# Kernel tuning notes

Measured on AMD Instinct MI355X. Metric: run time of the kernel, lower is better.

The kernel has to match this reference:

```python
import jax, jax.numpy as jnp
import numpy as np

B, T, HID = 4, 2048, 1024
H, D = 16, 64  # num_heads, depth = hidden // heads
NEG_INF = -1e9


def setup_inputs() -> dict:
    key = jax.random.key(0)
    ks = jax.random.split(key, 8)
    s = 1.0 / np.sqrt(HID)
    return {
        "q": jax.random.normal(ks[0], (B, T, HID), jnp.float32),
        "k": jax.random.normal(ks[1], (B, T, HID), jnp.float32),
        "v": jax.random.normal(ks[2], (B, T, HID), jnp.float32),
        "pad_mask": jax.random.randint(ks[3], (B, T), 0, 2, jnp.int32),
        "Wq": jax.random.normal(ks[4], (HID, HID), jnp.float32) * s,
        "Wk": jax.random.normal(ks[5], (HID, HID), jnp.float32) * s,
        "Wv": jax.random.normal(ks[6], (HID, HID), jnp.float32) * s,
        "Wo": jax.random.normal(ks[7], (HID, HID), jnp.float32) * s,
    }


def _split_heads(x):
    # [B, T, HID] -> [B*H, T, D]
    b, t, _ = x.shape
    return x.reshape(b, t, H, D).transpose(0, 2, 1, 3).reshape(b * H, t, D)


def _combine_heads(x):
    # [B*H, T, D] -> [B, T, HID]
    t = x.shape[1]
    return x.reshape(-1, H, t, D).transpose(0, 2, 1, 3).reshape(-1, t, HID)


def reference(q, k, v, pad_mask, Wq, Wk, Wv, Wo):
    qp = _split_heads(q @ Wq) * (D ** -0.5)   # [B*H, Tq, D]
    kp = _split_heads(k @ Wk)                  # [B*H, Tk, D]
    vp = _split_heads(v @ Wv)                  # [B*H, Tk, D]
    # additive pad bias: repeat([H,1]) is head-major tiling, reproduced via jnp.tile
    bias = jnp.tile(pad_mask.astype(jnp.float32) * NEG_INF, (H, 1))[:, None, :]
    logits = jnp.einsum('bqd,bkd->bqk', qp, kp) + bias  # [B*H, Tq, Tk]
    weights = jax.nn.softmax(logits, axis=-1)
    # original calls functional.dropout but discards the result -> no-op
    out = jnp.einsum('bqk,bkd->bqd', weights, vp)
    out = _combine_heads(out)                  # [B, Tq, HID]
    return out @ Wo
```

## Files before the change

### kernel.cpp

```cpp
#include <hip/hip_runtime.h>
#include <hip/hip_bf16.h>

#define TQ 2048
#define HIDDEN 1024
#define NB 4
#define NH 16
#define DH 64
#define BHN (NB*NH)
#define LOG2E 1.44269504f

typedef __attribute__((ext_vector_type(4))) float f32x4;
typedef __attribute__((ext_vector_type(8))) short s16x8;

#if __has_builtin(__builtin_amdgcn_exp2f)
#define EXP2(x) __builtin_amdgcn_exp2f(x)
#else
#define EXP2(x) exp2f(x)
#endif

__device__ inline unsigned short f2bf(float f) {
    union { float f; unsigned int u; } x; x.f = f;
    unsigned int r = x.u + 0x7fffu + ((x.u >> 16) & 1u);
    return (unsigned short)(r >> 16);
}

__device__ inline unsigned int pkbf(float a, float b) {
    __hip_bfloat162 h = __float22bfloat162_rn(make_float2(a, b));
    return *reinterpret_cast<unsigned int*>(&h);
}

union PBU { uint4 u4; s16x8 v; };

#define GLL16(gsrc, ldst) \
    __builtin_amdgcn_global_load_lds( \
        (const __attribute__((address_space(1))) unsigned int*)(gsrc), \
        (__attribute__((address_space(3))) unsigned int*)(ldst), 16, 0, 0)

__global__ __launch_bounds__(256) void maskprep(const int* __restrict__ pad,
                                                unsigned short* __restrict__ maskAndB) {
    int p = blockIdx.x * 256 + threadIdx.x;
    int r = p >> 11, off = p & 2047;
    int o6 = off & 63;
    int ks = o6 >> 5, k32 = o6 & 31;
    int lg = k32 >> 3, j = k32 & 7;
    int key = (off & ~63) | (ks * 32 + ((j >> 2) << 4) + (lg << 2) + (j & 3));
    maskAndB[p] = pad[r * 2048 + key] ? (unsigned short)0 : (unsigned short)0xFFFF;
}

__global__ __launch_bounds__(256) void wt_kernel(const float* W0, const float* W1,
                                                 const float* W2, const float* W3,
                                                 unsigned short* Wt) {
    const float* W = (blockIdx.z == 0) ? W0 : (blockIdx.z == 1) ? W1
                    : (blockIdx.z == 2) ? W2 : W3;
    unsigned short* out = Wt + (size_t)blockIdx.z * HIDDEN * HIDDEN;
    __shared__ float tile[64][68];
    int t = threadIdx.x;
    int k0 = blockIdx.y * 64, n0 = blockIdx.x * 64;
#pragma unroll
    for (int i = 0; i < 4; i++) {
        int r = (t >> 4) + i * 16;
        int c = (t & 15) * 4;
        float4 v = *(const float4*)(W + (size_t)(k0 + r) * HIDDEN + n0 + c);
        tile[r][c] = v.x; tile[r][c+1] = v.y; tile[r][c+2] = v.z; tile[r][c+3] = v.w;
    }
    __syncthreads();
#pragma unroll
    for (int i = 0; i < 4; i++) {
        int n = (t >> 4) + i * 16;
        int kc = (t & 15) * 4;
        ushort4 o;
        o.x = f2bf(tile[kc+0][n]); o.y = f2bf(tile[kc+1][n]);
        o.z = f2bf(tile[kc+2][n]); o.w = f2bf(tile[kc+3][n]);
        *(ushort4*)(out + (size_t)(n0 + n) * HIDDEN + k0 + kc) = o;
    }
}

__global__ __launch_bounds__(256) void gemm_proj(const float* __restrict__ A,
                                                 const unsigned short* __restrict__ Bt,
                                                 unsigned short* __restrict__ outb,
                                                 float scale, int vt) {
    __shared__ alignas(16) float As[128 * 32];
    __shared__ alignas(16) unsigned short Bs[128 * 32];
    const int t = threadIdx.x;
    const int wave = t >> 6, lane = t & 63;
    const int wr = wave >> 1, wc = wave & 1;
    const int lr = lane & 15, lg = lane >> 4;
    const int linear = blockIdx.x + 8 * blockIdx.y;
    const int tile = ((linear & 7) << 6) | (linear >> 3);
    const int m0 = (tile >> 3) * 128, n0 = (tile & 7) * 128;

    int fA[4]; size_t gA[4];
#pragma unroll
    for (int i = 0; i < 4; i++) {
        fA[i] = i * 256 + t;
        int row = fA[i] >> 3, sg = (fA[i] & 7) ^ (row & 7);
        gA[i] = (size_t)(m0 + row) * HIDDEN + sg * 4;
    }
    int fB[2]; size_t gB[2];
#pragma unroll
    for (int i = 0; i < 2; i++) {
        fB[i] = i * 256 + t;
        int row = fB[i] >> 2, sg = (fB[i] & 3) ^ (row & 3);
        gB[i] = (size_t)(n0 + row) * HIDDEN + sg * 8;
    }
    float* lA0 = &As[(size_t)(0 * 256 + wave * 64) * 4];
    float* lA1 = &As[(size_t)(1 * 256 + wave * 64) * 4];
    float* lA2 = &As[(size_t)(2 * 256 + wave * 64) * 4];
    float* lA3 = &As[(size_t)(3 * 256 + wave * 64) * 4];
    unsigned short* lB0 = &Bs[(size_t)(0 * 256 + wave * 64) * 8];
    unsigned short* lB1 = &Bs[(size_t)(1 * 256 + wave * 64) * 8];

    f32x4 acc[4][4] = {};

    for (int k0 = 0; k0 < HIDDEN; k0 += 32) {
        __syncthreads();
        GLL16(A + gA[0] + k0, lA0);
        GLL16(A + gA[1] + k0, lA1);
        GLL16(A + gA[2] + k0, lA2);
        GLL16(A + gA[3] + k0, lA3);
        GLL16(Bt + gB[0] + k0, lB0);
        GLL16(Bt + gB[1] + k0, lB1);
        __syncthreads();
        s16x8 af[4], bfr[4];
#pragma unroll
        for (int mi = 0; mi < 4; mi++) {
            int row = wr * 64 + mi * 16 + lr;
            int s0 = (lg * 2) ^ (row & 7), s1 = (lg * 2 + 1) ^ (row & 7);
            float4 a0 = *(const float4*)(&As[row * 32 + s0 * 4]);
            float4 a1 = *(const float4*)(&As[row * 32 + s1 * 4]);
            PBU u;
            u.u4.x = pkbf(a0.x, a0.y); u.u4.y = pkbf(a0.z, a0.w);
            u.u4.z = pkbf(a1.x, a1.y); u.u4.w = pkbf(a1.z, a1.w);
            af[mi] = u.v;
        }
#pragma unroll
        for (int ni = 0; ni < 4; ni++) {
            int row = wc * 64 + ni * 16 + lr;
            int s = lg ^ (row & 3);
            bfr[ni] = *(const s16x8*)(&Bs[row * 32 + s * 8]);
        }
#pragma unroll
        for (int mi = 0; mi < 4; mi++)
#pragma unroll
            for (int ni = 0; ni < 4; ni++)
                acc[mi][ni] = __builtin_amdgcn_mfma_f32_16x16x32_bf16(af[mi], bfr[ni], acc[mi][ni], 0, 0, 0);
    }

    if (vt == 0) {
#pragma unroll
        for (int mi = 0; mi < 4; mi++)
#pragma unroll
            for (int ni = 0; ni < 4; ni++)
#pragma unroll
                for (int j = 0; j < 4; j++) {
                    int m = m0 + wr * 64 + mi * 16 + lg * 4 + j;
                    int n = n0 + wc * 64 + ni * 16 + lr;
                    int b = m >> 11, tt = m & (TQ - 1);
                    int h = n >> 6, d = n & 63;
                    outb[((size_t)(b * NH + h) * TQ + tt) * DH + d] = f2bf(acc[mi][ni][j] * scale);
                }
    } else {
#pragma unroll
        for (int mi = 0; mi < 4; mi++)
#pragma unroll
            for (int ni = 0; ni < 4; ni++) {
                int m = m0 + wr * 64 + mi * 16 + lg * 4;
                int n = n0 + wc * 64 + ni * 16 + lr;
                int b = m >> 11, tt = m & (TQ - 1);
                int h = n >> 6, d = n & 63;
                ushort4 pk;
                pk.x = f2bf(acc[mi][ni][0] * scale);
                pk.y = f2bf(acc[mi][ni][1] * scale);
                pk.z = f2bf(acc[mi][ni][2] * scale);
                pk.w = f2bf(acc[mi][ni][3] * scale);
                *(ushort4*)(outb + ((size_t)(b * NH + h) * DH + d) * TQ + tt) = pk;
            }
    }
}

__global__ __launch_bounds__(256) void gemm_out(const unsigned short* __restrict__ A,
                                                const unsigned short* __restrict__ Bt,
                                                float* __restrict__ out) {
    __shared__ alignas(16) unsigned short As[128 * 32];
    __shared__ alignas(16) unsigned short Bs[128 * 32];
    const int t = threadIdx.x;
    const int wave = t >> 6, lane = t & 63;
    const int wr = wave >> 1, wc = wave & 1;
    const int lr = lane & 15, lg = lane >> 4;
    const int linear = blockIdx.x + 8 * blockIdx.y;
    const int tile = ((linear & 7) << 6) | (linear >> 3);
    const int m0 = (tile >> 3) * 128, n0 = (tile & 7) * 128;

    int fA[2]; size_t gA[2], gB[2];
#pragma unroll
    for (int i = 0; i < 2; i++) {
        fA[i] = i * 256 + t;
        int row = fA[i] >> 2, sg = (fA[i] & 3) ^ (row & 3);
        gA[i] = (size_t)(m0 + row) * HIDDEN + sg * 8;
        gB[i] = (size_t)(n0 + row) * HIDDEN + sg * 8;
    }
    unsigned short* lA0 = &As[(size_t)(0 * 256 + wave * 64) * 8];
    unsigned short* lA1 = &As[(size_t)(1 * 256 + wave * 64) * 8];
    unsigned short* lB0 = &Bs[(size_t)(0 * 256 + wave * 64) * 8];
    unsigned short* lB1 = &Bs[(size_t)(1 * 256 + wave * 64) * 8];

    f32x4 acc[4][4] = {};

    for (int k0 = 0; k0 < HIDDEN; k0 += 32) {
        __syncthreads();
        GLL16(A + gA[0] + k0, lA0);
        GLL16(A + gA[1] + k0, lA1);
        GLL16(Bt + gB[0] + k0, lB0);
        GLL16(Bt + gB[1] + k0, lB1);
        __syncthreads();
        s16x8 af[4], bfr[4];
#pragma unroll
        for (int mi = 0; mi < 4; mi++) {
            int row = wr * 64 + mi * 16 + lr;
            int s = lg ^ (row & 3);
            af[mi] = *(const s16x8*)(&As[row * 32 + s * 8]);
        }
#pragma unroll
        for (int ni = 0; ni < 4; ni++) {
            int row = wc * 64 + ni * 16 + lr;
            int s = lg ^ (row & 3);
            bfr[ni] = *(const s16x8*)(&Bs[row * 32 + s * 8]);
        }
#pragma unroll
        for (int mi = 0; mi < 4; mi++)
#pragma unroll
            for (int ni = 0; ni < 4; ni++)
                acc[mi][ni] = __builtin_amdgcn_mfma_f32_16x16x32_bf16(af[mi], bfr[ni], acc[mi][ni], 0, 0, 0);
    }
#pragma unroll
    for (int mi = 0; mi < 4; mi++)
#pragma unroll
        for (int ni = 0; ni < 4; ni++)
#pragma unroll
            for (int j = 0; j < 4; j++) {
                int m = m0 + wr * 64 + mi * 16 + lg * 4 + j;
                int n = n0 + wc * 64 + ni * 16 + lr;
                out[(size_t)m * HIDDEN + n] = acc[mi][ni][j];
            }
}

__global__ __launch_bounds__(512, 4) void attn_kernel(
        const unsigned short* __restrict__ QP,
        const unsigned short* __restrict__ KP,
        const unsigned short* __restrict__ VT,
        const unsigned short* __restrict__ maskAndB,
        unsigned short* __restrict__ AO) {
    __shared__ alignas(16) unsigned short Ks[2][64 * 72];
    __shared__ alignas(16) unsigned short Vs[2][64 * 72];
    const int t = threadIdx.x, wave = t >> 6, lane = t & 63;
    const int lr = lane & 15, lg = lane >> 4;
    const int linear = blockIdx.x + 8 * blockIdx.y;
    const int bh = ((linear & 7) << 3) | ((linear >> 3) & 7);
    const int qb = linear >> 6;
    const int q0 = qb * 256 + wave * 32;
    const unsigned short* Qb = QP + (size_t)bh * TQ * DH;
    const unsigned short* Kb = KP + (size_t)bh * TQ * DH;
    const unsigned short* Vb = VT + (size_t)bh * DH * TQ;
    const unsigned short* mrow = maskAndB + (bh & (NB - 1)) * TQ;

    const short ob = (short)0x3F80;
    const s16x8 ones = {ob, ob, ob, ob, ob, ob, ob, ob};

    s16x8 qf[2][2];
#pragma unroll
    for (int u = 0; u < 2; u++)
#pragma unroll
        for (int h = 0; h < 2; h++)
            qf[u][h] = *(const s16x8*)(Qb + (size_t)(q0 + u * 16 + lr) * DH + h * 32 + lg * 8);

    const int srow = t >> 3, scol = (t & 7) * 8;
    const unsigned short* kA = Kb + srow * DH + scol;
    const unsigned short* vA = Vb + (size_t)srow * TQ + scol;
    const int ksO = srow * 72 + scol;
    const int cc = t & 7;
    const int vg = ((cc & 4) << 1) + ((cc & 1) << 2) + ((cc >> 1) & 1);
    const int vO = srow * 72 + vg * 4;

    uint4 kr, vr;
#define LOAD_TILE(kt_) do { \
        kr = *(const uint4*)(kA + (size_t)(kt_) * 4096); \
        vr = *(const uint4*)(vA + (size_t)(kt_) * 64); \
    } while (0)
#define STORE_TILE(b_) do { \
        *(uint4*)(&Ks[b_][ksO]) = kr; \
        *(uint2*)(&Vs[b_][vO])     = make_uint2(vr.x, vr.y); \
        *(uint2*)(&Vs[b_][vO + 8]) = make_uint2(vr.z, vr.w); \
    } while (0)

    f32x4 o[2][4] = {};
    f32x4 osum[2] = {};

    LOAD_TILE(0);
    STORE_TILE(0);

    const int NT = TQ / 64;
    for (int kt = 0; kt < NT; kt++) {
        __syncthreads();
        const int cur = kt & 1;
        if (kt + 1 < NT) LOAD_TILE(kt + 1);
        uint4 ma0 = *(const uint4*)(mrow + kt * 64 + lg * 8);
        uint4 ma1 = *(const uint4*)(mrow + kt * 64 + 32 + lg * 8);

        f32x4 z[2][4] = {};
#pragma unroll
        for (int ni = 0; ni < 4; ni++) {
            s16x8 kf0 = *(const s16x8*)(&Ks[cur][(ni * 16 + lr) * 72 + lg * 8]);
            s16x8 kf1 = *(const s16x8*)(&Ks[cur][(ni * 16 + lr) * 72 + 32 + lg * 8]);
#pragma unroll
            for (int u = 0; u < 2; u++) {
                z[u][ni] = __builtin_amdgcn_mfma_f32_16x16x32_bf16(kf0, qf[u][0], z[u][ni], 0, 0, 0);
                z[u][ni] = __builtin_amdgcn_mfma_f32_16x16x32_bf16(kf1, qf[u][1], z[u][ni], 0, 0, 0);
            }
        }

        PBU pb[2][2];
#pragma unroll
        for (int u = 0; u < 2; u++) {
#pragma unroll
            for (int ni = 0; ni < 4; ni++)
#pragma unroll
                for (int r = 0; r < 4; r++)
                    z[u][ni][r] = EXP2(z[u][ni][r]);
#pragma unroll
            for (int ks = 0; ks < 2; ks++) {
                pb[u][ks].u4.x = pkbf(z[u][2 * ks][0], z[u][2 * ks][1]);
                pb[u][ks].u4.y = pkbf(z[u][2 * ks][2], z[u][2 * ks][3]);
                pb[u][ks].u4.z = pkbf(z[u][2 * ks + 1][0], z[u][2 * ks + 1][1]);
                pb[u][ks].u4.w = pkbf(z[u][2 * ks + 1][2], z[u][2 * ks + 1][3]);
            }
            pb[u][0].u4.x &= ma0.x; pb[u][0].u4.y &= ma0.y;
            pb[u][0].u4.z &= ma0.z; pb[u][0].u4.w &= ma0.w;
            pb[u][1].u4.x &= ma1.x; pb[u][1].u4.y &= ma1.y;
            pb[u][1].u4.z &= ma1.z; pb[u][1].u4.w &= ma1.w;
        }

#pragma unroll
        for (int di = 0; di < 4; di++)
#pragma unroll
            for (int ks = 0; ks < 2; ks++) {
                s16x8 vf = *(const s16x8*)(&Vs[cur][(di * 16 + lr) * 72 + ks * 32 + lg * 8]);
#pragma unroll
                for (int u = 0; u < 2; u++)
                    o[u][di] = __builtin_amdgcn_mfma_f32_16x16x32_bf16(vf, pb[u][ks].v, o[u][di], 0, 0, 0);
            }
#pragma unroll
        for (int u = 0; u < 2; u++) {
            osum[u] = __builtin_amdgcn_mfma_f32_16x16x32_bf16(ones, pb[u][0].v, osum[u], 0, 0, 0);
            osum[u] = __builtin_amdgcn_mfma_f32_16x16x32_bf16(ones, pb[u][1].v, osum[u], 0, 0, 0);
        }

        if (kt + 1 < NT) STORE_TILE((kt + 1) & 1);
    }

    const int b = bh >> 4, h = bh & 15;
#pragma unroll
    for (int u = 0; u < 2; u++) {
        float inv = 1.f / osum[u][0];
        int tt = q0 + u * 16 + lr;
#pragma unroll
        for (int di = 0; di < 4; di++) {
            uint2 w;
            w.x = pkbf(o[u][di][0] * inv, o[u][di][1] * inv);
            w.y = pkbf(o[u][di][2] * inv, o[u][di][3] * inv);
            *(uint2*)(AO + (size_t)(b * TQ + tt) * HIDDEN + h * 64 + di * 16 + lg * 4) = w;
        }
    }
#undef LOAD_TILE
#undef STORE_TILE
}

extern "C" void kernel_launch(void* const* d_in, const int* in_sizes, int n_in,
                              void* d_out, int out_size, void* d_ws, size_t ws_size,
                              hipStream_t stream) {
    const float* q  = (const float*)d_in[0];
    const float* k  = (const float*)d_in[1];
    const float* v  = (const float*)d_in[2];
    const int* pad  = (const int*)d_in[3];
    const float* Wq = (const float*)d_in[4];
    const float* Wk = (const float*)d_in[5];
    const float* Wv = (const float*)d_in[6];
    const float* Wo = (const float*)d_in[7];
    float* out = (float*)d_out;

    unsigned short* ws = (unsigned short*)d_ws;
    unsigned short* Wt = ws;
    unsigned short* AO = ws + (size_t)4 * 1024 * 1024;
    unsigned short* QP = AO + (size_t)BHN * TQ * DH;
    unsigned short* KP = QP + (size_t)BHN * TQ * DH;
    unsigned short* VTb = KP + (size_t)BHN * TQ * DH;
    unsigned short* maskAndB = VTb + (size_t)BHN * TQ * DH;
    (void)ws_size; (void)in_sizes; (void)n_in; (void)out_size;

    dim3 b256(256);
    const dim3 gGemm(8, 64);
    maskprep<<<dim3(NB * TQ / 256), b256, 0, stream>>>(pad, maskAndB);
    wt_kernel<<<dim3(16, 16, 4), b256, 0, stream>>>(Wq, Wk, Wv, Wo, Wt);
    gemm_proj<<<gGemm, b256, 0, stream>>>(q, Wt + (size_t)0 * 1024 * 1024, QP, 0.125f * LOG2E, 0);
    gemm_proj<<<gGemm, b256, 0, stream>>>(k, Wt + (size_t)1 * 1024 * 1024, KP, 1.0f, 0);
    gemm_proj<<<gGemm, b256, 0, stream>>>(v, Wt + (size_t)2 * 1024 * 1024, VTb, 1.0f, 1);
    attn_kernel<<<dim3(8, 64), dim3(512), 0, stream>>>(QP, KP, VTb, maskAndB, AO);
    gemm_out<<<gGemm, b256, 0, stream>>>(AO, Wt + (size_t)3 * 1024 * 1024, out);
}
```

Baseline: 221.9 us.

## Batch QKV projections into one launch and halve rows per attention wave

The three projection GEMMs are merged into a single launch with blockIdx.z picking the input, weight slice, output and scale. This removes launch gaps and lets the three GEMMs fill the GPU together. The attention kernel now gives each wave 16 query rows instead of 32 and doubles the grid to 1024 blocks. That raises parallelism and lowers register pressure, but each K/V tile loaded into shared memory is reused across half as many query rows, so K/V load traffic doubles.

```diff
diff --git a/kernel.cpp b/kernel.cpp
--- a/kernel.cpp
+++ b/kernel.cpp
@@ -75,10 +75,19 @@
     }
 }
 
-__global__ __launch_bounds__(256) void gemm_proj(const float* __restrict__ A,
-                                                 const unsigned short* __restrict__ Bt,
-                                                 unsigned short* __restrict__ outb,
-                                                 float scale, int vt) {
+__global__ __launch_bounds__(256) void gemm_proj(const float* __restrict__ Aq,
+                                                 const float* __restrict__ Ak,
+                                                 const float* __restrict__ Av,
+                                                 const unsigned short* __restrict__ Wt,
+                                                 unsigned short* __restrict__ QP,
+                                                 unsigned short* __restrict__ KP,
+                                                 unsigned short* __restrict__ VTb) {
+    const int zi = blockIdx.z;
+    const float* A = (zi == 0) ? Aq : (zi == 1) ? Ak : Av;
+    const unsigned short* Bt = Wt + (size_t)zi * HIDDEN * HIDDEN;
+    unsigned short* outb = (zi == 0) ? QP : (zi == 1) ? KP : VTb;
+    const float scale = (zi == 0) ? 0.125f * LOG2E : 1.0f;
+
     __shared__ alignas(16) float As[128 * 32];
     __shared__ alignas(16) unsigned short Bs[128 * 32];
     const int t = threadIdx.x;
@@ -89,18 +98,18 @@
     const int tile = ((linear & 7) << 6) | (linear >> 3);
     const int m0 = (tile >> 3) * 128, n0 = (tile & 7) * 128;
 
-    int fA[4]; size_t gA[4];
+    size_t gA[4];
 #pragma unroll
     for (int i = 0; i < 4; i++) {
-        fA[i] = i * 256 + t;
-        int row = fA[i] >> 3, sg = (fA[i] & 7) ^ (row & 7);
+        int f = i * 256 + t;
+        int row = f >> 3, sg = (f & 7) ^ (row & 7);
         gA[i] = (size_t)(m0 + row) * HIDDEN + sg * 4;
     }
-    int fB[2]; size_t gB[2];
+    size_t gB[2];
 #pragma unroll
     for (int i = 0; i < 2; i++) {
-        fB[i] = i * 256 + t;
-        int row = fB[i] >> 2, sg = (fB[i] & 3) ^ (row & 3);
+        int f = i * 256 + t;
+        int row = f >> 2, sg = (f & 3) ^ (row & 3);
         gB[i] = (size_t)(n0 + row) * HIDDEN + sg * 8;
     }
     float* lA0 = &As[(size_t)(0 * 256 + wave * 64) * 4];
@@ -146,7 +155,7 @@
                 acc[mi][ni] = __builtin_amdgcn_mfma_f32_16x16x32_bf16(af[mi], bfr[ni], acc[mi][ni], 0, 0, 0);
     }
 
-    if (vt == 0) {
+    if (zi != 2) {
 #pragma unroll
         for (int mi = 0; mi < 4; mi++)
 #pragma unroll
@@ -169,10 +178,10 @@
                 int b = m >> 11, tt = m & (TQ - 1);
                 int h = n >> 6, d = n & 63;
                 ushort4 pk;
-                pk.x = f2bf(acc[mi][ni][0] * scale);
-                pk.y = f2bf(acc[mi][ni][1] * scale);
-                pk.z = f2bf(acc[mi][ni][2] * scale);
-                pk.w = f2bf(acc[mi][ni][3] * scale);
+                pk.x = f2bf(acc[mi][ni][0]);
+                pk.y = f2bf(acc[mi][ni][1]);
+                pk.z = f2bf(acc[mi][ni][2]);
+                pk.w = f2bf(acc[mi][ni][3]);
                 *(ushort4*)(outb + ((size_t)(b * NH + h) * DH + d) * TQ + tt) = pk;
             }
     }
@@ -191,11 +200,11 @@
     const int tile = ((linear & 7) << 6) | (linear >> 3);
     const int m0 = (tile >> 3) * 128, n0 = (tile & 7) * 128;
 
-    int fA[2]; size_t gA[2], gB[2];
+    size_t gA[2], gB[2];
 #pragma unroll
     for (int i = 0; i < 2; i++) {
-        fA[i] = i * 256 + t;
-        int row = fA[i] >> 2, sg = (fA[i] & 3) ^ (row & 3);
+        int f = i * 256 + t;
+        int row = f >> 2, sg = (f & 3) ^ (row & 3);
         gA[i] = (size_t)(m0 + row) * HIDDEN + sg * 8;
         gB[i] = (size_t)(n0 + row) * HIDDEN + sg * 8;
     }
@@ -255,9 +264,10 @@
     const int t = threadIdx.x, wave = t >> 6, lane = t & 63;
     const int lr = lane & 15, lg = lane >> 4;
     const int linear = blockIdx.x + 8 * blockIdx.y;
-    const int bh = ((linear & 7) << 3) | ((linear >> 3) & 7);
-    const int qb = linear >> 6;
-    const int q0 = qb * 256 + wave * 32;
+    const int j = linear >> 3;
+    const int bh = ((linear & 7) << 3) | (j & 7);
+    const int qb = j >> 3;
+    const int q0 = qb * 128 + wave * 16;
     const unsigned short* Qb = QP + (size_t)bh * TQ * DH;
     const unsigned short* Kb = KP + (size_t)bh * TQ * DH;
     const unsigned short* Vb = VT + (size_t)bh * DH * TQ;
@@ -266,12 +276,8 @@
     const short ob = (short)0x3F80;
     const s16x8 ones = {ob, ob, ob, ob, ob, ob, ob, ob};
 
-    s16x8 qf[2][2];
-#pragma unroll
-    for (int u = 0; u < 2; u++)
-#pragma unroll
-        for (int h = 0; h < 2; h++)
-            qf[u][h] = *(const s16x8*)(Qb + (size_t)(q0 + u * 16 + lr) * DH + h * 32 + lg * 8);
+    s16x8 qf0 = *(const s16x8*)(Qb + (size_t)(q0 + lr) * DH + lg * 8);
+    s16x8 qf1 = *(const s16x8*)(Qb + (size_t)(q0 + lr) * DH + 32 + lg * 8);
 
     const int srow = t >> 3, scol = (t & 7) * 8;
     const unsigned short* kA = Kb + srow * DH + scol;
@@ -292,8 +298,8 @@
         *(uint2*)(&Vs[b_][vO + 8]) = make_uint2(vr.z, vr.w); \
     } while (0)
 
-    f32x4 o[2][4] = {};
-    f32x4 osum[2] = {};
+    f32x4 o[4] = {};
+    f32x4 osum = {};
 
     LOAD_TILE(0);
     STORE_TILE(0);
@@ -306,69 +312,55 @@
         uint4 ma0 = *(const uint4*)(mrow + kt * 64 + lg * 8);
         uint4 ma1 = *(const uint4*)(mrow + kt * 64 + 32 + lg * 8);
 
-        f32x4 z[2][4] = {};
+        f32x4 z[4] = {};
 #pragma unroll
         for (int ni = 0; ni < 4; ni++) {
             s16x8 kf0 = *(const s16x8*)(&Ks[cur][(ni * 16 + lr) * 72 + lg * 8]);
             s16x8 kf1 = *(const s16x8*)(&Ks[cur][(ni * 16 + lr) * 72 + 32 + lg * 8]);
-#pragma unroll
-            for (int u = 0; u < 2; u++) {
-                z[u][ni] = __builtin_amdgcn_mfma_f32_16x16x32_bf16(kf0, qf[u][0], z[u][ni], 0, 0, 0);
-                z[u][ni] = __builtin_amdgcn_mfma_f32_16x16x32_bf16(kf1, qf[u][1], z[u][ni], 0, 0, 0);
-            }
-        }
-
-        PBU pb[2][2];
-#pragma unroll
-        for (int u = 0; u < 2; u++) {
-#pragma unroll
-            for (int ni = 0; ni < 4; ni++)
-#pragma unroll
-                for (int r = 0; r < 4; r++)
-                    z[u][ni][r] = EXP2(z[u][ni][r]);
-#pragma unroll
-            for (int ks = 0; ks < 2; ks++) {
-                pb[u][ks].u4.x = pkbf(z[u][2 * ks][0], z[u][2 * ks][1]);
-                pb[u][ks].u4.y = pkbf(z[u][2 * ks][2], z[u][2 * ks][3]);
-                pb[u][ks].u4.z = pkbf(z[u][2 * ks + 1][0], z[u][2 * ks + 1][1]);
-                pb[u][ks].u4.w = pkbf(z[u][2 * ks + 1][2], z[u][2 * ks + 1][3]);
-            }
-            pb[u][0].u4.x &= ma0.x; pb[u][0].u4.y &= ma0.y;
-            pb[u][0].u4.z &= ma0.z; pb[u][0].u4.w &= ma0.w;
-            pb[u][1].u4.x &= ma1.x; pb[u][1].u4.y &= ma1.y;
-            pb[u][1].u4.z &= ma1.z; pb[u][1].u4.w &= ma1.w;
-        }
+            z[ni] = __builtin_amdgcn_mfma_f32_16x16x32_bf16(kf0, qf0, z[ni], 0, 0, 0);
+            z[ni] = __builtin_amdgcn_mfma_f32_16x16x32_bf16(kf1, qf1, z[ni], 0, 0, 0);
+        }
+
+#pragma unroll
+        for (int ni = 0; ni < 4; ni++)
+#pragma unroll
+            for (int r = 0; r < 4; r++)
+                z[ni][r] = EXP2(z[ni][r]);
+        PBU pb[2];
+#pragma unroll
+        for (int ks = 0; ks < 2; ks++) {
+            pb[ks].u4.x = pkbf(z[2 * ks][0], z[2 * ks][1]);
+            pb[ks].u4.y = pkbf(z[2 * ks][2], z[2 * ks][3]);
+            pb[ks].u4.z = pkbf(z[2 * ks + 1][0], z[2 * ks + 1][1]);
+            pb[ks].u4.w = pkbf(z[2 * ks + 1][2], z[2 * ks + 1][3]);
+        }
+        pb[0].u4.x &= ma0.x; pb[0].u4.y &= ma0.y;
+        pb[0].u4.z &= ma0.z; pb[0].u4.w &= ma0.w;
+        pb[1].u4.x &= ma1.x; pb[1].u4.y &= ma1.y;
+        pb[1].u4.z &= ma1.z; pb[1].u4.w &= ma1.w;
 
 #pragma unroll
         for (int di = 0; di < 4; di++)
 #pragma unroll
             for (int ks = 0; ks < 2; ks++) {
                 s16x8 vf = *(const s16x8*)(&Vs[cur][(di * 16 + lr) * 72 + ks * 32 + lg * 8]);
-#pragma unroll
-                for (int u = 0; u < 2; u++)
-                    o[u][di] = __builtin_amdgcn_mfma_f32_16x16x32_bf16(vf, pb[u][ks].v, o[u][di], 0, 0, 0);
+                o[di] = __builtin_amdgcn_mfma_f32_16x16x32_bf16(vf, pb[ks].v, o[di], 0, 0, 0);
             }
-#pragma unroll
-        for (int u = 0; u < 2; u++) {
-            osum[u] = __builtin_amdgcn_mfma_f32_16x16x32_bf16(ones, pb[u][0].v, osum[u], 0, 0, 0);
-            osum[u] = __builtin_amdgcn_mfma_f32_16x16x32_bf16(ones, pb[u][1].v, osum[u], 0, 0, 0);
-        }
+        osum = __builtin_amdgcn_mfma_f32_16x16x32_bf16(ones, pb[0].v, osum, 0, 0, 0);
+        osum = __builtin_amdgcn_mfma_f32_16x16x32_bf16(ones, pb[1].v, osum, 0, 0, 0);
 
         if (kt + 1 < NT) STORE_TILE((kt + 1) & 1);
     }
 
     const int b = bh >> 4, h = bh & 15;
-#pragma unroll
-    for (int u = 0; u < 2; u++) {
-        float inv = 1.f / osum[u][0];
-        int tt = q0 + u * 16 + lr;
-#pragma unroll
-        for (int di = 0; di < 4; di++) {
-            uint2 w;
-            w.x = pkbf(o[u][di][0] * inv, o[u][di][1] * inv);
-            w.y = pkbf(o[u][di][2] * inv, o[u][di][3] * inv);
-            *(uint2*)(AO + (size_t)(b * TQ + tt) * HIDDEN + h * 64 + di * 16 + lg * 4) = w;
-        }
+    float inv = 1.f / osum[0];
+    int tt = q0 + lr;
+#pragma unroll
+    for (int di = 0; di < 4; di++) {
+        uint2 w;
+        w.x = pkbf(o[di][0] * inv, o[di][1] * inv);
+        w.y = pkbf(o[di][2] * inv, o[di][3] * inv);
+        *(uint2*)(AO + (size_t)(b * TQ + tt) * HIDDEN + h * 64 + di * 16 + lg * 4) = w;
     }
 #undef LOAD_TILE
 #undef STORE_TILE
@@ -397,12 +389,9 @@
     (void)ws_size; (void)in_sizes; (void)n_in; (void)out_size;
 
     dim3 b256(256);
-    const dim3 gGemm(8, 64);
     maskprep<<<dim3(NB * TQ / 256), b256, 0, stream>>>(pad, maskAndB);
     wt_kernel<<<dim3(16, 16, 4), b256, 0, stream>>>(Wq, Wk, Wv, Wo, Wt);
-    gemm_proj<<<gGemm, b256, 0, stream>>>(q, Wt + (size_t)0 * 1024 * 1024, QP, 0.125f * LOG2E, 0);
-    gemm_proj<<<gGemm, b256, 0, stream>>>(k, Wt + (size_t)1 * 1024 * 1024, KP, 1.0f, 0);
-    gemm_proj<<<gGemm, b256, 0, stream>>>(v, Wt + (size_t)2 * 1024 * 1024, VTb, 1.0f, 1);
-    attn_kernel<<<dim3(8, 64), dim3(512), 0, stream>>>(QP, KP, VTb, maskAndB, AO);
-    gemm_out<<<gGemm, b256, 0, stream>>>(AO, Wt + (size_t)3 * 1024 * 1024, out);
-}
+    gemm_proj<<<dim3(8, 64, 3), b256, 0, stream>>>(q, k, v, Wt, QP, KP, VTb);
+    attn_kernel<<<dim3(8, 128), dim3(512), 0, stream>>>(QP, KP, VTb, maskAndB, AO);
+    gemm_out<<<dim3(8, 64), b256, 0, stream>>>(AO, Wt + (size_t)3 * 1024 * 1024, out);
+}
```

Measured after the change: 245.1 us. +10.4%, slower.

## Load K/V MFMA fragments directly from global memory, dropping LDS staging

Applied to the files above, without the earlier changes.

The attention kernel no longer stages K and V tiles through double-buffered shared memory with barriers. Each wave now reads its MFMA fragments straight from global memory, relying on L1/L2 caching since all 8 waves read the same tiles. To allow contiguous V fragment loads, the V-projection epilogue permutes the token index within 32-token groups so that it matches the fragment layout. s_setprio hints are also placed around the MFMA sections. This removes LDS traffic and syncs but adds redundant global/cache loads per wave and exposes their latency without explicit prefetch.

```diff
diff --git a/kernel.cpp b/kernel.cpp
--- a/kernel.cpp
+++ b/kernel.cpp
@@ -89,18 +89,18 @@
     const int tile = ((linear & 7) << 6) | (linear >> 3);
     const int m0 = (tile >> 3) * 128, n0 = (tile & 7) * 128;
 
-    int fA[4]; size_t gA[4];
+    size_t gA[4];
 #pragma unroll
     for (int i = 0; i < 4; i++) {
-        fA[i] = i * 256 + t;
-        int row = fA[i] >> 3, sg = (fA[i] & 7) ^ (row & 7);
+        int f = i * 256 + t;
+        int row = f >> 3, sg = (f & 7) ^ (row & 7);
         gA[i] = (size_t)(m0 + row) * HIDDEN + sg * 4;
     }
-    int fB[2]; size_t gB[2];
+    size_t gB[2];
 #pragma unroll
     for (int i = 0; i < 2; i++) {
-        fB[i] = i * 256 + t;
-        int row = fB[i] >> 2, sg = (fB[i] & 3) ^ (row & 3);
+        int f = i * 256 + t;
+        int row = f >> 2, sg = (f & 3) ^ (row & 3);
         gB[i] = (size_t)(n0 + row) * HIDDEN + sg * 8;
     }
     float* lA0 = &As[(size_t)(0 * 256 + wave * 64) * 4];
@@ -168,12 +168,13 @@
                 int n = n0 + wc * 64 + ni * 16 + lr;
                 int b = m >> 11, tt = m & (TQ - 1);
                 int h = n >> 6, d = n & 63;
+                int ttp = (tt & ~31) | (lg << 3) | ((mi & 1) << 2);
                 ushort4 pk;
                 pk.x = f2bf(acc[mi][ni][0] * scale);
                 pk.y = f2bf(acc[mi][ni][1] * scale);
                 pk.z = f2bf(acc[mi][ni][2] * scale);
                 pk.w = f2bf(acc[mi][ni][3] * scale);
-                *(ushort4*)(outb + ((size_t)(b * NH + h) * DH + d) * TQ + tt) = pk;
+                *(ushort4*)(outb + ((size_t)(b * NH + h) * DH + d) * TQ + ttp) = pk;
             }
     }
 }
@@ -191,11 +192,11 @@
     const int tile = ((linear & 7) << 6) | (linear >> 3);
     const int m0 = (tile >> 3) * 128, n0 = (tile & 7) * 128;
 
-    int fA[2]; size_t gA[2], gB[2];
+    size_t gA[2], gB[2];
 #pragma unroll
     for (int i = 0; i < 2; i++) {
-        fA[i] = i * 256 + t;
-        int row = fA[i] >> 2, sg = (fA[i] & 3) ^ (row & 3);
+        int f = i * 256 + t;
+        int row = f >> 2, sg = (f & 3) ^ (row & 3);
         gA[i] = (size_t)(m0 + row) * HIDDEN + sg * 8;
         gB[i] = (size_t)(n0 + row) * HIDDEN + sg * 8;
     }
@@ -250,8 +251,6 @@
         const unsigned short* __restrict__ VT,
         const unsigned short* __restrict__ maskAndB,
         unsigned short* __restrict__ AO) {
-    __shared__ alignas(16) unsigned short Ks[2][64 * 72];
-    __shared__ alignas(16) unsigned short Vs[2][64 * 72];
     const int t = threadIdx.x, wave = t >> 6, lane = t & 63;
     const int lr = lane & 15, lg = lane >> 4;
     const int linear = blockIdx.x + 8 * blockIdx.y;
@@ -273,50 +272,38 @@
         for (int h = 0; h < 2; h++)
             qf[u][h] = *(const s16x8*)(Qb + (size_t)(q0 + u * 16 + lr) * DH + h * 32 + lg * 8);
 
-    const int srow = t >> 3, scol = (t & 7) * 8;
-    const unsigned short* kA = Kb + srow * DH + scol;
-    const unsigned short* vA = Vb + (size_t)srow * TQ + scol;
-    const int ksO = srow * 72 + scol;
-    const int cc = t & 7;
-    const int vg = ((cc & 4) << 1) + ((cc & 1) << 2) + ((cc >> 1) & 1);
-    const int vO = srow * 72 + vg * 4;
-
-    uint4 kr, vr;
-#define LOAD_TILE(kt_) do { \
-        kr = *(const uint4*)(kA + (size_t)(kt_) * 4096); \
-        vr = *(const uint4*)(vA + (size_t)(kt_) * 64); \
-    } while (0)
-#define STORE_TILE(b_) do { \
-        *(uint4*)(&Ks[b_][ksO]) = kr; \
-        *(uint2*)(&Vs[b_][vO])     = make_uint2(vr.x, vr.y); \
-        *(uint2*)(&Vs[b_][vO + 8]) = make_uint2(vr.z, vr.w); \
-    } while (0)
+    const unsigned short* kB[4];
+#pragma unroll
+    for (int ni = 0; ni < 4; ni++)
+        kB[ni] = Kb + (size_t)(ni * 16 + lr) * DH + lg * 8;
+    const unsigned short* vB[4];
+#pragma unroll
+    for (int di = 0; di < 4; di++)
+        vB[di] = Vb + (size_t)(di * 16 + lr) * TQ + lg * 8;
+    const unsigned short* mB = mrow + lg * 8;
 
     f32x4 o[2][4] = {};
     f32x4 osum[2] = {};
 
-    LOAD_TILE(0);
-    STORE_TILE(0);
-
     const int NT = TQ / 64;
     for (int kt = 0; kt < NT; kt++) {
-        __syncthreads();
-        const int cur = kt & 1;
-        if (kt + 1 < NT) LOAD_TILE(kt + 1);
-        uint4 ma0 = *(const uint4*)(mrow + kt * 64 + lg * 8);
-        uint4 ma1 = *(const uint4*)(mrow + kt * 64 + 32 + lg * 8);
+        const int kOff = kt * 64 * DH;
+        const int vOff = kt * 64;
+        uint4 ma0 = *(const uint4*)(mB + vOff);
+        uint4 ma1 = *(const uint4*)(mB + vOff + 32);
 
         f32x4 z[2][4] = {};
+        __builtin_amdgcn_s_setprio(1);
 #pragma unroll
         for (int ni = 0; ni < 4; ni++) {
-            s16x8 kf0 = *(const s16x8*)(&Ks[cur][(ni * 16 + lr) * 72 + lg * 8]);
-            s16x8 kf1 = *(const s16x8*)(&Ks[cur][(ni * 16 + lr) * 72 + 32 + lg * 8]);
-#pragma unroll
-            for (int u = 0; u < 2; u++) {
-                z[u][ni] = __builtin_amdgcn_mfma_f32_16x16x32_bf16(kf0, qf[u][0], z[u][ni], 0, 0, 0);
-                z[u][ni] = __builtin_amdgcn_mfma_f32_16x16x32_bf16(kf1, qf[u][1], z[u][ni], 0, 0, 0);
-            }
-        }
+            s16x8 kf0 = *(const s16x8*)(kB[ni] + kOff);
+            s16x8 kf1 = *(const s16x8*)(kB[ni] + kOff + 32);
+            z[0][ni] = __builtin_amdgcn_mfma_f32_16x16x32_bf16(kf0, qf[0][0], z[0][ni], 0, 0, 0);
+            z[0][ni] = __builtin_amdgcn_mfma_f32_16x16x32_bf16(kf1, qf[0][1], z[0][ni], 0, 0, 0);
+            z[1][ni] = __builtin_amdgcn_mfma_f32_16x16x32_bf16(kf0, qf[1][0], z[1][ni], 0, 0, 0);
+            z[1][ni] = __builtin_amdgcn_mfma_f32_16x16x32_bf16(kf1, qf[1][1], z[1][ni], 0, 0, 0);
+        }
+        __builtin_amdgcn_s_setprio(0);
 
         PBU pb[2][2];
 #pragma unroll
@@ -339,22 +326,22 @@
             pb[u][1].u4.z &= ma1.z; pb[u][1].u4.w &= ma1.w;
         }
 
-#pragma unroll
-        for (int di = 0; di < 4; di++)
-#pragma unroll
-            for (int ks = 0; ks < 2; ks++) {
-                s16x8 vf = *(const s16x8*)(&Vs[cur][(di * 16 + lr) * 72 + ks * 32 + lg * 8]);
-#pragma unroll
-                for (int u = 0; u < 2; u++)
-                    o[u][di] = __builtin_amdgcn_mfma_f32_16x16x32_bf16(vf, pb[u][ks].v, o[u][di], 0, 0, 0);
-            }
+        __builtin_amdgcn_s_setprio(1);
+#pragma unroll
+        for (int di = 0; di < 4; di++) {
+            s16x8 vf0 = *(const s16x8*)(vB[di] + vOff);
+            s16x8 vf1 = *(const s16x8*)(vB[di] + vOff + 32);
+            o[0][di] = __builtin_amdgcn_mfma_f32_16x16x32_bf16(vf0, pb[0][0].v, o[0][di], 0, 0, 0);
+            o[0][di] = __builtin_amdgcn_mfma_f32_16x16x32_bf16(vf1, pb[0][1].v, o[0][di], 0, 0, 0);
+            o[1][di] = __builtin_amdgcn_mfma_f32_16x16x32_bf16(vf0, pb[1][0].v, o[1][di], 0, 0, 0);
+            o[1][di] = __builtin_amdgcn_mfma_f32_16x16x32_bf16(vf1, pb[1][1].v, o[1][di], 0, 0, 0);
+        }
 #pragma unroll
         for (int u = 0; u < 2; u++) {
             osum[u] = __builtin_amdgcn_mfma_f32_16x16x32_bf16(ones, pb[u][0].v, osum[u], 0, 0, 0);
             osum[u] = __builtin_amdgcn_mfma_f32_16x16x32_bf16(ones, pb[u][1].v, osum[u], 0, 0, 0);
         }
-
-        if (kt + 1 < NT) STORE_TILE((kt + 1) & 1);
+        __builtin_amdgcn_s_setprio(0);
     }
 
     const int b = bh >> 4, h = bh & 15;
@@ -370,8 +357,6 @@
             *(uint2*)(AO + (size_t)(b * TQ + tt) * HIDDEN + h * 64 + di * 16 + lg * 4) = w;
         }
     }
-#undef LOAD_TILE
-#undef STORE_TILE
 }
 
 extern "C" void kernel_launch(void* const* d_in, const int* in_sizes, int n_in,
```

Result: slower. 382.2 us (+72.2%).
